# Optimization experiments

Measured on AMD Instinct MI355X. Metric: run time of the kernel, lower is better.

The kernel has to match this reference:

```python
import jax, jax.numpy as jnp
import numpy as np

N_NODES = 50000
N_EDGES = 1600000
IN_DIM = 128
HID = 64
N_GRAPHS = 256


def gcn_conv(x, row, col, W, b, n_nodes):
    """PyG GCNConv: symmetric gcn_norm with self-loops, linear-then-aggregate."""
    h = x @ W  # [N, out]
    loop = jnp.arange(n_nodes, dtype=row.dtype)
    r = jnp.concatenate([row, loop])  # sources (messages from x[r])
    c = jnp.concatenate([col, loop])  # targets (aggregate at c)
    ew = jnp.ones(r.shape[0], dtype=x.dtype)
    deg = jax.ops.segment_sum(ew, c, num_segments=n_nodes)
    dinv = jnp.where(deg > 0, jax.lax.rsqrt(deg), 0.0).astype(x.dtype)
    norm = dinv[r] * dinv[c]  # [E+N]
    out = jax.ops.segment_sum(norm[:, None] * h[r], c, num_segments=n_nodes)
    return out + b


def global_mean_pool(x, batch, n_graphs):
    sums = jax.ops.segment_sum(x, batch, num_segments=n_graphs)
    cnt = jax.ops.segment_sum(jnp.ones(x.shape[0], x.dtype), batch, num_segments=n_graphs)
    return sums / jnp.clip(cnt, 1.0)[:, None]


def setup_inputs() -> dict:
    key = jax.random.key(0)
    ks = jax.random.split(key, 12)
    x = jax.random.normal(ks[0], (N_NODES, IN_DIM), dtype=jnp.float32)
    edge_index = jax.random.randint(ks[1], (2, N_EDGES), 0, N_NODES, dtype=jnp.int64)
    batch = jnp.sort(jax.random.randint(ks[2], (N_NODES,), 0, N_GRAPHS, dtype=jnp.int64))
    def glorot(k, shp):
        lim = float(np.sqrt(6.0 / (shp[0] + shp[1])))
        return jax.random.uniform(k, shp, jnp.float32, -lim, lim)
    return {
        "x": x,
        "edge_index": edge_index,
        "batch": batch,
        "W1": glorot(ks[3], (IN_DIM, HID)), "b1": jnp.zeros((HID,), jnp.float32),
        "W2": glorot(ks[4], (HID, HID)), "b2": jnp.zeros((HID,), jnp.float32),
        "W3": glorot(ks[5], (HID, HID)), "b3": jnp.zeros((HID,), jnp.float32),
        "Wl1": glorot(ks[6], (HID, 16)), "bl1": jnp.zeros((16,), jnp.float32),
        "Wl2": glorot(ks[7], (16, 1)), "bl2": jnp.zeros((1,), jnp.float32),
    }


def reference(x, edge_index, batch, W1, b1, W2, b2, W3, b3, Wl1, bl1, Wl2, bl2):
    n = x.shape[0]
    row, col = edge_index[0], edge_index[1]
    h = jax.nn.relu(gcn_conv(x, row, col, W1, b1, n))
    h = jax.nn.relu(gcn_conv(h, row, col, W2, b2, n))
    h = jax.nn.relu(gcn_conv(h, row, col, W3, b3, n))
    g = global_mean_pool(h, batch, N_GRAPHS)  # [G, 64]
    out = (g @ Wl1 + bl1) @ Wl2 + bl2  # [G, 1]
    return out
```

## Files before the change

### kernel.cpp

```cpp
#include <hip/hip_runtime.h>

#define HID 64
#define B1 256
#define NBMAX 200
#define CAP 10368

typedef __attribute__((ext_vector_type(8))) short short8;
typedef __attribute__((ext_vector_type(4))) float float4v;

__device__ __forceinline__ ushort f2bf(float f) {
  unsigned u = __float_as_uint(f);
  unsigned r = (u + 0x7fffu + ((u >> 16) & 1u)) >> 16;
  return (ushort)r;
}
__device__ __forceinline__ float bf2f(ushort v) {
  return __uint_as_float(((unsigned)v) << 16);
}
__device__ __forceinline__ float4 up4(ushort4 v) {
  float4 r;
  r.x = bf2f(v.x);
  r.y = bf2f(v.y);
  r.z = bf2f(v.z);
  r.w = bf2f(v.w);
  return r;
}


__global__ __launch_bounds__(256) void bucket_hist(const int* __restrict__ col, int E, int epb,
                                                   int nb, int* __restrict__ blockcnt) {
  __shared__ int cnt[NBMAX];
  int b = blockIdx.x, t = threadIdx.x;
  for (int i = t; i < nb; i += 256) cnt[i] = 0;
  __syncthreads();
  int lo = b * epb, hi = min(lo + epb, E);
  for (int e = lo + t; e < hi; e += 256) atomicAdd(&cnt[col[e] >> 8], 1);
  __syncthreads();
  for (int i = t; i < nb; i += 256) blockcnt[i * B1 + b] = cnt[i];
}

__global__ __launch_bounds__(256) void scan_blockcnt(int* __restrict__ blockcnt,
                                                     int* __restrict__ buckettot) {
  __shared__ int s[256];
  int k = blockIdx.x, t = threadIdx.x;
  int v = blockcnt[k * B1 + t];
  s[t] = v;
  __syncthreads();
  for (int d = 1; d < 256; d <<= 1) {
    int u = (t >= d) ? s[t - d] : 0;
    __syncthreads();
    s[t] += u;
    __syncthreads();
  }
  blockcnt[k * B1 + t] = s[t] - v;
  if (t == 255) buckettot[k] = s[255];
}

__global__ __launch_bounds__(256) void scan_buckettot(const int* __restrict__ buckettot,
                                                      int* __restrict__ bucketbase,
                                                      int* __restrict__ csr_off, int n, int E,
                                                      int nb) {
  __shared__ int s[256];
  int t = threadIdx.x;
  int v = (t < nb) ? buckettot[t] : 0;
  s[t] = v;
  __syncthreads();
  for (int d = 1; d < 256; d <<= 1) {
    int u = (t >= d) ? s[t - d] : 0;
    __syncthreads();
    s[t] += u;
    __syncthreads();
  }
  if (t <= nb) bucketbase[t] = (t == 0) ? 0 : s[t - 1];
  if (t == 0) csr_off[n] = E;
}

__global__ __launch_bounds__(256) void bin_edges(const int* __restrict__ row,
                                                 const int* __restrict__ col, int E, int epb,
                                                 int nb, const int* __restrict__ blockcnt,
                                                 const int* __restrict__ bucketbase,
                                                 unsigned* __restrict__ binned) {
  __shared__ int woff[NBMAX];
  int b = blockIdx.x, t = threadIdx.x;
  for (int i = t; i < nb; i += 256) woff[i] = blockcnt[i * B1 + b] + bucketbase[i];
  __syncthreads();
  int lo = b * epb, hi = min(lo + epb, E);
  for (int e = lo + t; e < hi; e += 256) {
    int c = col[e];
    int r = row[e];
    int pos = atomicAdd(&woff[c >> 8], 1);
    binned[pos] = ((unsigned)r << 8) | (unsigned)(c & 255);
  }
}

__global__ __launch_bounds__(256) void bucket_csr(const unsigned* __restrict__ binned,
                                                  const int* __restrict__ bucketbase,
                                                  int* __restrict__ csr_off,
                                                  int* __restrict__ csr_src,
                                                  float* __restrict__ dinv, int n) {
  __shared__ int lcnt[256];
  __shared__ int lofs[256];
  __shared__ int lsrc[CAP];
  int k = blockIdx.x, t = threadIdx.x;
  int base = bucketbase[k], end = bucketbase[k + 1];
  int s = end - base;
  lcnt[t] = 0;
  __syncthreads();
  for (int i = t; i < s; i += 256) {
    unsigned p = binned[base + i];
    atomicAdd(&lcnt[p & 255u], 1);
  }
  __syncthreads();
  int v = lcnt[t];
  lofs[t] = v;
  __syncthreads();
  for (int d = 1; d < 256; d <<= 1) {
    int u = (t >= d) ? lofs[t - d] : 0;
    __syncthreads();
    lofs[t] += u;
    __syncthreads();
  }
  int excl = lofs[t] - v;
  int node = (k << 8) + t;
  if (node < n) {
    csr_off[node] = base + excl;
    dinv[node] = rsqrtf((float)(v + 1));
  }
  lcnt[t] = excl;
  __syncthreads();
  for (int i = t; i < s; i += 256) {
    unsigned p = binned[base + i];
    int pos = atomicAdd(&lcnt[p & 255u], 1);
    if (pos < CAP) lsrc[pos] = (int)(p >> 8);
  }
  __syncthreads();
  for (int i = t; i < s; i += 256) csr_src[base + i] = (i < CAP) ? lsrc[i] : 0;
}


__global__ __launch_bounds__(256) void prep_w(const float* __restrict__ W1,
                                              const float* __restrict__ W2,
                                              const float* __restrict__ W3,
                                              ushort* __restrict__ Wt1h, ushort* __restrict__ Wt1l,
                                              ushort* __restrict__ Wt2h, ushort* __restrict__ Wt2l,
                                              ushort* __restrict__ Wt3h, ushort* __restrict__ Wt3l) {
  int t = blockIdx.x * 256 + threadIdx.x;
  if (t < 128 * 64) {
    int k = t >> 6, nn = t & 63;
    float w = W1[t];
    ushort h = f2bf(w);
    Wt1h[nn * 128 + k] = h;
    Wt1l[nn * 128 + k] = f2bf(w - bf2f(h));
  }
  if (t < 64 * 64) {
    int k = t >> 6, nn = t & 63;
    float w2 = W2[t], w3 = W3[t];
    ushort h2 = f2bf(w2), h3 = f2bf(w3);
    Wt2h[nn * 64 + k] = h2;
    Wt2l[nn * 64 + k] = f2bf(w2 - bf2f(h2));
    Wt3h[nn * 64 + k] = h3;
    Wt3l[nn * 64 + k] = f2bf(w3 - bf2f(h3));
  }
}


template <int K>
__global__ __launch_bounds__(256) void gemm_mfma(const float* __restrict__ A,
                                                 const ushort* __restrict__ Wh,
                                                 const ushort* __restrict__ Wl,
                                                 const float* __restrict__ dinv,
                                                 ushort* __restrict__ out, int n) {
  int wave = (blockIdx.x * 256 + threadIdx.x) >> 6;
  int lane = threadIdx.x & 63;
  int row0 = wave * 16;
  if (row0 >= n) return;
  int m = lane & 15;
  int quad = lane >> 4;
  int r = row0 + m;
  int rc = (r < n) ? r : (n - 1);

  float4v acc[4];
#pragma unroll
  for (int t = 0; t < 4; ++t) acc[t] = (float4v){0.f, 0.f, 0.f, 0.f};

#pragma unroll
  for (int k0 = 0; k0 < K; k0 += 32) {
    const float4* xp = (const float4*)&A[(size_t)rc * K + k0 + quad * 8];
    float4 a0 = xp[0];
    float4 a1 = xp[1];
    float av[8] = {a0.x, a0.y, a0.z, a0.w, a1.x, a1.y, a1.z, a1.w};
    short8 ah, al;
#pragma unroll
    for (int i = 0; i < 8; ++i) {
      ushort h = f2bf(av[i]);
      ah[i] = (short)h;
      al[i] = (short)f2bf(av[i] - bf2f(h));
    }
#pragma unroll
    for (int t = 0; t < 4; ++t) {
      size_t wof = (size_t)(t * 16 + m) * K + k0 + quad * 8;
      short8 bh = *(const short8*)&Wh[wof];
      short8 bl = *(const short8*)&Wl[wof];
      acc[t] = __builtin_amdgcn_mfma_f32_16x16x32_bf16(ah, bh, acc[t], 0, 0, 0);
      acc[t] = __builtin_amdgcn_mfma_f32_16x16x32_bf16(al, bh, acc[t], 0, 0, 0);
      acc[t] = __builtin_amdgcn_mfma_f32_16x16x32_bf16(ah, bl, acc[t], 0, 0, 0);
    }
  }

  float4 dv = ((const float4*)dinv)[(row0 >> 2) + quad];
  float dvi[4] = {dv.x, dv.y, dv.z, dv.w};
#pragma unroll
  for (int i = 0; i < 4; ++i) {
    int orow = row0 + quad * 4 + i;
    if (orow < n) {
#pragma unroll
      for (int t = 0; t < 4; ++t) {
        out[(size_t)orow * 64 + t * 16 + m] = f2bf(dvi[i] * acc[t][i]);
      }
    }
  }
}


__global__ __launch_bounds__(256) void agg_kernel(
    const ushort* __restrict__ hs, const int* __restrict__ csr_off,
    const int* __restrict__ csr_src, const float* __restrict__ dinv,
    const float* __restrict__ bias, float* __restrict__ out, int n) {
  int wid = (blockIdx.x * 256 + threadIdx.x) >> 6;
  int lane = threadIdx.x & 63;
  if (wid >= n) return;
  int qe = lane >> 4;
  int fq = lane & 15;
  const ushort4* hs4 = (const ushort4*)hs;

  float4 acc = make_float4(0.f, 0.f, 0.f, 0.f);
  if (qe == 0) {
    float4 s = up4(hs4[(size_t)wid * 16 + fq]);
    acc.x += s.x; acc.y += s.y; acc.z += s.z; acc.w += s.w;
  }

  int j = csr_off[wid];
  int e = csr_off[wid + 1];

  int pre = min(e, (j + 3) & ~3);
  if (j + qe < pre) {
    int s0 = csr_src[j + qe];
    float4 f = up4(hs4[(size_t)s0 * 16 + fq]);
    acc.x += f.x; acc.y += f.y; acc.z += f.z; acc.w += f.w;
  }
  int base = pre;

  for (; base + 16 <= e; base += 16) {
    int4 s = *(const int4*)&csr_src[base + qe * 4];
    float4 f0 = up4(hs4[(size_t)s.x * 16 + fq]);
    float4 f1 = up4(hs4[(size_t)s.y * 16 + fq]);
    float4 f2 = up4(hs4[(size_t)s.z * 16 + fq]);
    float4 f3 = up4(hs4[(size_t)s.w * 16 + fq]);
    acc.x += f0.x + f1.x + f2.x + f3.x;
    acc.y += f0.y + f1.y + f2.y + f3.y;
    acc.z += f0.z + f1.z + f2.z + f3.z;
    acc.w += f0.w + f1.w + f2.w + f3.w;
  }

  for (; base + 4 <= e; base += 4) {
    int s0 = csr_src[base + qe];
    float4 f = up4(hs4[(size_t)s0 * 16 + fq]);
    acc.x += f.x; acc.y += f.y; acc.z += f.z; acc.w += f.w;
  }
  if (base + qe < e) {
    int s0 = csr_src[base + qe];
    float4 f = up4(hs4[(size_t)s0 * 16 + fq]);
    acc.x += f.x; acc.y += f.y; acc.z += f.z; acc.w += f.w;
  }

  acc.x += __shfl_xor(acc.x, 16, 64);
  acc.y += __shfl_xor(acc.y, 16, 64);
  acc.z += __shfl_xor(acc.z, 16, 64);
  acc.w += __shfl_xor(acc.w, 16, 64);
  acc.x += __shfl_xor(acc.x, 32, 64);
  acc.y += __shfl_xor(acc.y, 32, 64);
  acc.z += __shfl_xor(acc.z, 32, 64);
  acc.w += __shfl_xor(acc.w, 32, 64);

  if (qe == 0) {
    float d = dinv[wid];
    float4 bi = ((const float4*)bias)[fq];
    float4 r;
    r.x = fmaxf(d * acc.x + bi.x, 0.f);
    r.y = fmaxf(d * acc.y + bi.y, 0.f);
    r.z = fmaxf(d * acc.z + bi.z, 0.f);
    r.w = fmaxf(d * acc.w + bi.w, 0.f);
    ((float4*)out)[(size_t)wid * 16 + fq] = r;
  }
}


__global__ __launch_bounds__(256) void pool_mlp_kernel(
    const float* __restrict__ a, const int* __restrict__ batch, int n,
    const float* __restrict__ Wl1, const float* __restrict__ bl1,
    const float* __restrict__ Wl2, const float* __restrict__ bl2,
    float* __restrict__ out) {
  int g = blockIdx.x;
  int t = threadIdx.x;
  int lane = t & 63;
  int w = t >> 6;

  int lo = 0, hi = n;
  while (lo < hi) {
    int m = (lo + hi) >> 1;
    if (batch[m] < g) lo = m + 1; else hi = m;
  }
  int start = lo;
  lo = start; hi = n;
  while (lo < hi) {
    int m = (lo + hi) >> 1;
    if (batch[m] < g + 1) lo = m + 1; else hi = m;
  }
  int end = lo;

  float s = 0.f;
  for (int i = start + w; i < end; i += 4) s += a[i * 64 + lane];

  __shared__ float ps[4][64];
  __shared__ float gv[64];
  __shared__ float hv[16];
  ps[w][lane] = s;
  __syncthreads();
  if (w == 0) {
    float tot = ps[0][lane] + ps[1][lane] + ps[2][lane] + ps[3][lane];
    gv[lane] = tot / (float)max(end - start, 1);
  }
  __syncthreads();
  if (t < 16) {
    float h = bl1[t];
    for (int k = 0; k < 64; ++k) h += gv[k] * Wl1[k * 16 + t];
    hv[t] = h;
  }
  __syncthreads();
  if (t == 0) {
    float o = bl2[0];
    for (int j2 = 0; j2 < 16; ++j2) o += hv[j2] * Wl2[j2];
    out[g] = o;
  }
}


extern "C" void kernel_launch(void* const* d_in, const int* in_sizes, int n_in,
                              void* d_out, int out_size, void* d_ws, size_t ws_size,
                              hipStream_t stream) {
  const float* x = (const float*)d_in[0];
  const int* ei = (const int*)d_in[1];
  const int* batch = (const int*)d_in[2];
  const float* W1 = (const float*)d_in[3];
  const float* b1 = (const float*)d_in[4];
  const float* W2 = (const float*)d_in[5];
  const float* b2 = (const float*)d_in[6];
  const float* W3 = (const float*)d_in[7];
  const float* b3 = (const float*)d_in[8];
  const float* Wl1 = (const float*)d_in[9];
  const float* bl1 = (const float*)d_in[10];
  const float* Wl2 = (const float*)d_in[11];
  const float* bl2 = (const float*)d_in[12];

  int n = in_sizes[0] / 128;
  int E = in_sizes[1] / 2;
  int G = out_size;
  int nb = (n + 255) >> 8;
  int epb = (E + B1 - 1) / B1;

  const int* row = ei;
  const int* col = ei + E;

  char* p = (char*)d_ws;
  int* blockcnt = (int*)p;    p += (size_t)NBMAX * B1 * 4;
  int* buckettot = (int*)p;   p += 256 * 4;
  int* bucketbase = (int*)p;  p += 256 * 4;
  int* csr_off = (int*)p;     p += 50064 * 4;
  float* dinv = (float*)p;    p += 50016 * 4;
  ushort* Wt1h = (ushort*)p;  p += 128 * 64 * 2;
  ushort* Wt1l = (ushort*)p;  p += 128 * 64 * 2;
  ushort* Wt2h = (ushort*)p;  p += 64 * 64 * 2;
  ushort* Wt2l = (ushort*)p;  p += 64 * 64 * 2;
  ushort* Wt3h = (ushort*)p;  p += 64 * 64 * 2;
  ushort* Wt3l = (ushort*)p;  p += 64 * 64 * 2;
  int* csr_src = (int*)p;     p += (size_t)((E + 15) / 16 * 16) * 4;
  ushort* hs = (ushort*)p;    p += (size_t)n * 64 * 2;
  float* abuf = (float*)p;
  unsigned* binned = (unsigned*)hs;

  bucket_hist<<<B1, 256, 0, stream>>>(col, E, epb, nb, blockcnt);
  scan_blockcnt<<<nb, 256, 0, stream>>>(blockcnt, buckettot);
  scan_buckettot<<<1, 256, 0, stream>>>(buckettot, bucketbase, csr_off, n, E, nb);
  bin_edges<<<B1, 256, 0, stream>>>(row, col, E, epb, nb, blockcnt, bucketbase, binned);
  prep_w<<<32, 256, 0, stream>>>(W1, W2, W3, Wt1h, Wt1l, Wt2h, Wt2l, Wt3h, Wt3l);
  bucket_csr<<<nb, 256, 0, stream>>>(binned, bucketbase, csr_off, csr_src, dinv, n);

  int nwaves = (n + 15) / 16;
  int gblocks = (nwaves + 3) / 4;
  int ablocks = (n * 64 + 255) / 256;

  gemm_mfma<128><<<gblocks, 256, 0, stream>>>(x, Wt1h, Wt1l, dinv, hs, n);
  agg_kernel<<<ablocks, 256, 0, stream>>>(hs, csr_off, csr_src, dinv, b1, abuf, n);
  gemm_mfma<64><<<gblocks, 256, 0, stream>>>(abuf, Wt2h, Wt2l, dinv, hs, n);
  agg_kernel<<<ablocks, 256, 0, stream>>>(hs, csr_off, csr_src, dinv, b2, abuf, n);
  gemm_mfma<64><<<gblocks, 256, 0, stream>>>(abuf, Wt3h, Wt3l, dinv, hs, n);
  agg_kernel<<<ablocks, 256, 0, stream>>>(hs, csr_off, csr_src, dinv, b3, abuf, n);
  pool_mlp_kernel<<<G, 256, 0, stream>>>(abuf, batch, n, Wl1, bl1, Wl2, bl2, (float*)d_out);
}
```

Measured before the change: 334.5 us.

## Restructure edge binning with atomic bucket offsets and shared-memory staged writes

Replaces the per-block histogram plus block-count scan with global atomic bucket totals, and drops the scan_blockcnt kernel. bin_edges now takes chunks of 4096 edges, sorts each chunk by bucket in shared memory, reserves contiguous ranges with global atomics, and writes them out as runs rather than scattered stores. The weight prep is folded into bucket_hist, which removes a launch. Edge order inside a bucket becomes nondeterministic. The packed encoding now assumes node ids fit in 16 bits, which holds for 50000 nodes.

```diff
diff --git a/kernel.cpp b/kernel.cpp
--- a/kernel.cpp
+++ b/kernel.cpp
@@ -27,36 +27,45 @@
 
 
 __global__ __launch_bounds__(256) void bucket_hist(const int* __restrict__ col, int E, int epb,
-                                                   int nb, int* __restrict__ blockcnt) {
-  __shared__ int cnt[NBMAX];
+                                                   int* __restrict__ buckettot,
+                                                   const float* __restrict__ W1,
+                                                   const float* __restrict__ W2,
+                                                   const float* __restrict__ W3,
+                                                   ushort* __restrict__ Wt1h, ushort* __restrict__ Wt1l,
+                                                   ushort* __restrict__ Wt2h, ushort* __restrict__ Wt2l,
+                                                   ushort* __restrict__ Wt3h, ushort* __restrict__ Wt3l) {
   int b = blockIdx.x, t = threadIdx.x;
-  for (int i = t; i < nb; i += 256) cnt[i] = 0;
+  int gt = b * 256 + t;
+  if (gt < 128 * 64) {
+    int k = gt >> 6, nn = gt & 63;
+    float w = W1[gt];
+    ushort h = f2bf(w);
+    Wt1h[nn * 128 + k] = h;
+    Wt1l[nn * 128 + k] = f2bf(w - bf2f(h));
+  }
+  if (gt < 64 * 64) {
+    int k = gt >> 6, nn = gt & 63;
+    float w2 = W2[gt], w3 = W3[gt];
+    ushort h2 = f2bf(w2), h3 = f2bf(w3);
+    Wt2h[nn * 64 + k] = h2;
+    Wt2l[nn * 64 + k] = f2bf(w2 - bf2f(h2));
+    Wt3h[nn * 64 + k] = h3;
+    Wt3l[nn * 64 + k] = f2bf(w3 - bf2f(h3));
+  }
+
+  __shared__ int cnt[256];
+  cnt[t] = 0;
   __syncthreads();
   int lo = b * epb, hi = min(lo + epb, E);
   for (int e = lo + t; e < hi; e += 256) atomicAdd(&cnt[col[e] >> 8], 1);
   __syncthreads();
-  for (int i = t; i < nb; i += 256) blockcnt[i * B1 + b] = cnt[i];
-}
-
-__global__ __launch_bounds__(256) void scan_blockcnt(int* __restrict__ blockcnt,
-                                                     int* __restrict__ buckettot) {
-  __shared__ int s[256];
-  int k = blockIdx.x, t = threadIdx.x;
-  int v = blockcnt[k * B1 + t];
-  s[t] = v;
-  __syncthreads();
-  for (int d = 1; d < 256; d <<= 1) {
-    int u = (t >= d) ? s[t - d] : 0;
-    __syncthreads();
-    s[t] += u;
-    __syncthreads();
-  }
-  blockcnt[k * B1 + t] = s[t] - v;
-  if (t == 255) buckettot[k] = s[255];
+  int v = cnt[t];
+  if (v > 0) atomicAdd(&buckettot[t], v);
 }
 
 __global__ __launch_bounds__(256) void scan_buckettot(const int* __restrict__ buckettot,
                                                       int* __restrict__ bucketbase,
+                                                      int* __restrict__ woffglob,
                                                       int* __restrict__ csr_off, int n, int E,
                                                       int nb) {
   __shared__ int s[256];
@@ -70,25 +79,60 @@
     s[t] += u;
     __syncthreads();
   }
-  if (t <= nb) bucketbase[t] = (t == 0) ? 0 : s[t - 1];
+  int base = (t == 0) ? 0 : s[t - 1];
+  if (t <= nb) bucketbase[t] = base;
+  woffglob[t] = base;
   if (t == 0) csr_off[n] = E;
 }
 
 __global__ __launch_bounds__(256) void bin_edges(const int* __restrict__ row,
                                                  const int* __restrict__ col, int E, int epb,
-                                                 int nb, const int* __restrict__ blockcnt,
-                                                 const int* __restrict__ bucketbase,
+                                                 int* __restrict__ woffglob,
                                                  unsigned* __restrict__ binned) {
-  __shared__ int woff[NBMAX];
+  __shared__ int cnt[256];
+  __shared__ int ofs[256];
+  __shared__ int gb[256];
+  __shared__ int lcur[256];
+  __shared__ unsigned stage[4096];
   int b = blockIdx.x, t = threadIdx.x;
-  for (int i = t; i < nb; i += 256) woff[i] = blockcnt[i * B1 + b] + bucketbase[i];
-  __syncthreads();
   int lo = b * epb, hi = min(lo + epb, E);
-  for (int e = lo + t; e < hi; e += 256) {
-    int c = col[e];
-    int r = row[e];
-    int pos = atomicAdd(&woff[c >> 8], 1);
-    binned[pos] = ((unsigned)r << 8) | (unsigned)(c & 255);
+
+  for (int bs = lo; bs < hi; bs += 4096) {
+    int ecnt = min(4096, hi - bs);
+    cnt[t] = 0;
+    __syncthreads();
+    for (int i = t; i < ecnt; i += 256) atomicAdd(&cnt[col[bs + i] >> 8], 1);
+    __syncthreads();
+    int v = cnt[t];
+    ofs[t] = v;
+    __syncthreads();
+    for (int d = 1; d < 256; d <<= 1) {
+      int u = (t >= d) ? ofs[t - d] : 0;
+      __syncthreads();
+      ofs[t] += u;
+      __syncthreads();
+    }
+    int excl = ofs[t] - v;
+    int g = 0;
+    if (v > 0) g = atomicAdd(&woffglob[t], v);
+    __syncthreads();
+    ofs[t] = excl;
+    gb[t] = g;
+    lcur[t] = excl;
+    __syncthreads();
+    for (int i = t; i < ecnt; i += 256) {
+      int c = col[bs + i];
+      int r = row[bs + i];
+      int p = atomicAdd(&lcur[c >> 8], 1);
+      stage[p] = ((unsigned)r << 16) | (unsigned)c;
+    }
+    __syncthreads();
+    for (int i = t; i < ecnt; i += 256) {
+      unsigned en = stage[i];
+      int bb = (en >> 8) & 255;
+      binned[gb[bb] + (i - ofs[bb])] = en;
+    }
+    __syncthreads();
   }
 }
 
@@ -130,36 +174,10 @@
   for (int i = t; i < s; i += 256) {
     unsigned p = binned[base + i];
     int pos = atomicAdd(&lcnt[p & 255u], 1);
-    if (pos < CAP) lsrc[pos] = (int)(p >> 8);
+    if (pos < CAP) lsrc[pos] = (int)(p >> 16);
   }
   __syncthreads();
   for (int i = t; i < s; i += 256) csr_src[base + i] = (i < CAP) ? lsrc[i] : 0;
-}
-
-
-__global__ __launch_bounds__(256) void prep_w(const float* __restrict__ W1,
-                                              const float* __restrict__ W2,
-                                              const float* __restrict__ W3,
-                                              ushort* __restrict__ Wt1h, ushort* __restrict__ Wt1l,
-                                              ushort* __restrict__ Wt2h, ushort* __restrict__ Wt2l,
-                                              ushort* __restrict__ Wt3h, ushort* __restrict__ Wt3l) {
-  int t = blockIdx.x * 256 + threadIdx.x;
-  if (t < 128 * 64) {
-    int k = t >> 6, nn = t & 63;
-    float w = W1[t];
-    ushort h = f2bf(w);
-    Wt1h[nn * 128 + k] = h;
-    Wt1l[nn * 128 + k] = f2bf(w - bf2f(h));
-  }
-  if (t < 64 * 64) {
-    int k = t >> 6, nn = t & 63;
-    float w2 = W2[t], w3 = W3[t];
-    ushort h2 = f2bf(w2), h3 = f2bf(w3);
-    Wt2h[nn * 64 + k] = h2;
-    Wt2l[nn * 64 + k] = f2bf(w2 - bf2f(h2));
-    Wt3h[nn * 64 + k] = h3;
-    Wt3l[nn * 64 + k] = f2bf(w3 - bf2f(h3));
-  }
 }
 
 
@@ -371,9 +389,9 @@
   const int* col = ei + E;
 
   char* p = (char*)d_ws;
-  int* blockcnt = (int*)p;    p += (size_t)NBMAX * B1 * 4;
   int* buckettot = (int*)p;   p += 256 * 4;
-  int* bucketbase = (int*)p;  p += 256 * 4;
+  int* bucketbase = (int*)p;  p += 272 * 4;
+  int* woffglob = (int*)p;    p += 256 * 4;
   int* csr_off = (int*)p;     p += 50064 * 4;
   float* dinv = (float*)p;    p += 50016 * 4;
   ushort* Wt1h = (ushort*)p;  p += 128 * 64 * 2;
@@ -387,11 +405,11 @@
   float* abuf = (float*)p;
   unsigned* binned = (unsigned*)hs;
 
-  bucket_hist<<<B1, 256, 0, stream>>>(col, E, epb, nb, blockcnt);
-  scan_blockcnt<<<nb, 256, 0, stream>>>(blockcnt, buckettot);
-  scan_buckettot<<<1, 256, 0, stream>>>(buckettot, bucketbase, csr_off, n, E, nb);
-  bin_edges<<<B1, 256, 0, stream>>>(row, col, E, epb, nb, blockcnt, bucketbase, binned);
-  prep_w<<<32, 256, 0, stream>>>(W1, W2, W3, Wt1h, Wt1l, Wt2h, Wt2l, Wt3h, Wt3l);
+  hipMemsetAsync(buckettot, 0, 256 * 4, stream);
+  bucket_hist<<<B1, 256, 0, stream>>>(col, E, epb, buckettot,
+                                      W1, W2, W3, Wt1h, Wt1l, Wt2h, Wt2l, Wt3h, Wt3l);
+  scan_buckettot<<<1, 256, 0, stream>>>(buckettot, bucketbase, woffglob, csr_off, n, E, nb);
+  bin_edges<<<B1, 256, 0, stream>>>(row, col, E, epb, woffglob, binned);
   bucket_csr<<<nb, 256, 0, stream>>>(binned, bucketbase, csr_off, csr_src, dinv, n);
 
   int nwaves = (n + 15) / 16;
```

Result: no change. 332.1 us (-0.7%).
